# Kernel tuning notes

Measured on AMD Instinct MI355X. Metric: run time of the kernel, lower is better.

## Reference

```python
import jax, jax.numpy as jnp
import numpy as np

B, L, DIM = 16, 1024, 768
HEADS, DIM_HEAD = 12, 64
INNER = HEADS * DIM_HEAD  # 768


def _make_perm(key, l, dim):
    # first `dim` entries identity, rest a random permutation of [dim, l*dim)
    tail = dim + jax.random.permutation(key, (l - 1) * dim)
    return jnp.concatenate([jnp.arange(dim), tail]).astype(jnp.int32)


def setup_inputs() -> dict:
    key = jax.random.key(0)
    kx, kq, kk, kv, ko, kp1, kp2 = jax.random.split(key, 7)
    s = DIM ** -0.5
    return {
        "x": jax.random.normal(kx, (B, L, DIM), dtype=jnp.float32),
        "Wq": jax.random.normal(kq, (DIM, INNER), dtype=jnp.float32) * s,
        "Wk": jax.random.normal(kk, (DIM, INNER), dtype=jnp.float32) * s,
        "Wv": jax.random.normal(kv, (DIM, INNER), dtype=jnp.float32) * s,
        "Wo": jax.random.normal(ko, (INNER, DIM), dtype=jnp.float32) * (INNER ** -0.5),
        "bo": jnp.zeros((DIM,), dtype=jnp.float32),
        "permq": _make_perm(kp1, L, DIM),
        "permk": _make_perm(kp2, L, DIM),
    }


def reference(x, Wq, Wk, Wv, Wo, bo, permq, permk):
    b, l, d = x.shape
    scale = DIM_HEAD ** -0.5
    flat = x.reshape(b, l * d)
    xq = flat[:, permq].reshape(b, l, d)  # irregular gather across (seq*dim)
    xk = flat[:, permk].reshape(b, l, d)
    # projections + head split: b n (h d) -> b h n d
    q = (xq @ Wq).reshape(b, l, HEADS, DIM_HEAD).transpose(0, 2, 1, 3)
    k = (xk @ Wk).reshape(b, l, HEADS, DIM_HEAD).transpose(0, 2, 1, 3)
    v = (x @ Wv).reshape(b, l, HEADS, DIM_HEAD).transpose(0, 2, 1, 3)
    dots = jnp.einsum('bhnd,bhmd->bhnm', q, k) * scale
    attn = jax.nn.softmax(dots, axis=-1)
    out = jnp.einsum('bhnm,bhmd->bhnd', attn, v)
    out = out.transpose(0, 2, 1, 3).reshape(b, l, INNER)
    return out @ Wo + bo
```

## Files before the change

kernel.cpp:

```cpp
#include <hip/hip_runtime.h>

typedef unsigned short u16;
typedef __attribute__((ext_vector_type(8))) short bf16x8;
typedef __attribute__((ext_vector_type(4))) float f32x4;
typedef __attribute__((ext_vector_type(16))) float f32x16;

#define MFMA16(a, b, c) __builtin_amdgcn_mfma_f32_16x16x32_bf16(a, b, c, 0, 0, 0)
#define MFMA32(a, b, c) __builtin_amdgcn_mfma_f32_32x32x16_bf16(a, b, c, 0, 0, 0)

#if defined(__has_builtin)
# if __has_builtin(__builtin_amdgcn_cvt_pk_bf16_f32)
#  define HAS_CVT_PK 1
# else
#  define HAS_CVT_PK 0
# endif
#else
# define HAS_CVT_PK 0
#endif

__device__ __forceinline__ u16 f2b(float f) {
    union { float f; unsigned int u; } v;
    v.f = f;
    unsigned int u = v.u;
    return (u16)((u + 0x7fffu + ((u >> 16) & 1u)) >> 16);
}

__device__ __forceinline__ unsigned int f2b_pk(float a, float b) {
#if HAS_CVT_PK
    auto r = __builtin_amdgcn_cvt_pk_bf16_f32(a, b);
    unsigned int u;
    __builtin_memcpy(&u, &r, 4);
    return u;
#else
    return (unsigned int)f2b(a) | ((unsigned int)f2b(b) << 16);
#endif
}

__device__ __forceinline__ unsigned int cvtpk_asm(float a, float b) {
    unsigned int r;
    asm("v_cvt_pk_bf16_f32 %0, %1, %2" : "=v"(r) : "v"(a), "v"(b));
    return r;
}

__device__ __forceinline__ void g2l16(const u16* gsrc, u16* ldst) {
    __builtin_amdgcn_global_load_lds(
        (const __attribute__((address_space(1))) void*)gsrc,
        (__attribute__((address_space(3))) void*)ldst,
        16, 0, 0);
}

__global__ __launch_bounds__(256) void prep_weights(
    const float* __restrict__ Wq, const float* __restrict__ Wk,
    const float* __restrict__ Wv, const float* __restrict__ Wo,
    u16* __restrict__ wqt, u16* __restrict__ wkt,
    u16* __restrict__ wvt, u16* __restrict__ wot) {
    int id = blockIdx.x * 256 + threadIdx.x;
    int k = id / 768, n = id % 768;
    int t = n * 768 + k;
    wqt[t] = f2b(Wq[id] * (0.125f * 1.44269504088896340736f));
    wkt[t] = f2b(Wk[id]);
    wvt[t] = f2b(Wv[id]);
    wot[t] = f2b(Wo[id]);
}

__global__ __launch_bounds__(256) void cast_transpose(
    const float* __restrict__ x, u16* __restrict__ xb, u16* __restrict__ xT) {
    __shared__ __attribute__((aligned(16))) u16 T[16 * 1032];
    int t = threadIdx.x;
    int j0 = blockIdx.x * 1024;
#pragma unroll
    for (int b = 0; b < 16; ++b) {
        float4 v = *(const float4*)&x[(size_t)b * 786432 + j0 + 4 * t];
        uint2 o = make_uint2(f2b_pk(v.x, v.y), f2b_pk(v.z, v.w));
        *(uint2*)&T[b * 1032 + 4 * t] = o;
        *(uint2*)&xb[(size_t)b * 786432 + j0 + 4 * t] = o;
    }
    __syncthreads();
#pragma unroll
    for (int p = 0; p < 4; ++p) {
        int jl = t + 256 * p;
        union { u16 u[16]; int4 v[2]; } r;
#pragma unroll
        for (int b = 0; b < 16; ++b) r.u[b] = T[b * 1032 + jl];
        size_t base = (size_t)(j0 + jl) * 16;
        *(int4*)&xT[base] = r.v[0];
        *(int4*)&xT[base + 8] = r.v[1];
    }
}

__global__ __launch_bounds__(256) void gather_untranspose(
    const u16* __restrict__ xT, const int* __restrict__ permq,
    const int* __restrict__ permk, u16* __restrict__ dstQ,
    u16* __restrict__ dstK) {
    __shared__ u16 T[16 * 1034];
    const int* perm = blockIdx.y ? permk : permq;
    u16* dst = blockIdx.y ? dstK : dstQ;
    int t = threadIdx.x;
    int j0 = blockIdx.x * 1024;
#pragma unroll
    for (int p = 0; p < 4; ++p) {
        int jl = p * 256 + t;
        int pq = perm[j0 + jl];
        union { u16 u[16]; int4 v[2]; } r;
        const int4* s = (const int4*)&xT[(size_t)pq * 16];
        r.v[0] = s[0];
        r.v[1] = s[1];
#pragma unroll
        for (int b = 0; b < 16; ++b) T[b * 1034 + jl] = r.u[b];
    }
    __syncthreads();
#pragma unroll
    for (int b = 0; b < 16; ++b) {
        const unsigned int* s = (const unsigned int*)&T[b * 1034 + 4 * t];
        uint2 o = make_uint2(s[0], s[1]);
        *(uint2*)&dst[(size_t)b * 786432 + j0 + 4 * t] = o;
    }
}

__device__ __forceinline__ void gemm_core(
    const u16* __restrict__ A, const u16* __restrict__ Bt,
    u16* __restrict__ Cb, float* __restrict__ Cf,
    const float* __restrict__ bias, int m0, int n0, int K, int N, int mode) {
    __shared__ __attribute__((aligned(16))) u16 As[128 * 64];
    __shared__ __attribute__((aligned(16))) u16 Bs[128 * 64];
    int tid = threadIdx.x;
    int wave = tid >> 6, lane = tid & 63;
    int lo = lane & 15, quad = lane >> 4;
    int wm = (wave >> 1) * 64, wn = (wave & 1) * 64;
    f32x4 acc[4][4] = {};

    const u16* pA[4];
    const u16* pB[4];
    u16* lA[4];
    u16* lB[4];
#pragma unroll
    for (int p = 0; p < 4; ++p) {
        int c = p * 256 + wave * 64 + lane;
        int row = c >> 3;
        int scol = ((c & 7) ^ (row & 7)) * 8;
        pA[p] = A + (size_t)(m0 + row) * K + scol;
        pB[p] = Bt + (size_t)(n0 + row) * K + scol;
        lA[p] = &As[(p * 256 + wave * 64) * 8];
        lB[p] = &Bs[(p * 256 + wave * 64) * 8];
    }

    for (int k0 = 0; k0 < K; k0 += 64) {
        __syncthreads();
#pragma unroll
        for (int p = 0; p < 4; ++p) g2l16(pA[p], lA[p]);
#pragma unroll
        for (int p = 0; p < 4; ++p) g2l16(pB[p], lB[p]);
#pragma unroll
        for (int p = 0; p < 4; ++p) { pA[p] += 64; pB[p] += 64; }
        __syncthreads();
#pragma unroll
        for (int kk = 0; kk < 2; ++kk) {
            bf16x8 af[4], bf[4];
#pragma unroll
            for (int mi = 0; mi < 4; ++mi) {
                int row = wm + mi * 16 + lo;
                af[mi] = *(const bf16x8*)&As[row * 64 + (((kk << 2) | quad) ^ (lo & 7)) * 8];
            }
#pragma unroll
            for (int nj = 0; nj < 4; ++nj) {
                int row = wn + nj * 16 + lo;
                bf[nj] = *(const bf16x8*)&Bs[row * 64 + (((kk << 2) | quad) ^ (lo & 7)) * 8];
            }
#pragma unroll
            for (int mi = 0; mi < 4; ++mi)
#pragma unroll
                for (int nj = 0; nj < 4; ++nj)
                    acc[mi][nj] = MFMA16(af[mi], bf[nj], acc[mi][nj]);
        }
    }
#pragma unroll
    for (int mi = 0; mi < 4; ++mi)
#pragma unroll
        for (int nj = 0; nj < 4; ++nj) {
            int col = n0 + wn + nj * 16 + lo;
#pragma unroll
            for (int r = 0; r < 4; ++r) {
                int row = m0 + wm + mi * 16 + quad * 4 + r;
                float v = acc[mi][nj][r];
                if (mode) Cf[(size_t)row * N + col] = v + bias[col];
                else      Cb[(size_t)row * N + col] = f2b(v);
            }
        }
}

__global__ __launch_bounds__(256) void gemm_qkv(
    const u16* __restrict__ xqb, const u16* __restrict__ wqt, u16* __restrict__ Qb,
    const u16* __restrict__ xkb, const u16* __restrict__ wkt, u16* __restrict__ Kb,
    const u16* __restrict__ xb,  const u16* __restrict__ wvt, u16* __restrict__ Vb) {
    int id = blockIdx.x;
    int xcd = id & 7, slot = id >> 3;
    int gi = slot / 6, j = slot % 6;
    int group = xcd + 8 * gi;
    int my = group & 127, z = group >> 7;
    const u16* A = (z == 0) ? xqb : (z == 1) ? xkb : xb;
    const u16* W = (z == 0) ? wqt : (z == 1) ? wkt : wvt;
    u16* C = (z == 0) ? Qb : (z == 1) ? Kb : Vb;
    gemm_core(A, W, C, nullptr, nullptr, my * 128, j * 128, 768, 768, 0);
}

__global__ __launch_bounds__(256) void gemm_out(
    const u16* __restrict__ A, const u16* __restrict__ Bt,
    float* __restrict__ Cf, const float* __restrict__ bias) {
    int id = blockIdx.x;
    int xcd = id & 7, slot = id >> 3;
    int gi = slot / 6, j = slot % 6;
    int group = xcd + 8 * gi;
    gemm_core(A, Bt, nullptr, Cf, bias, group * 128, j * 128, 768, 768, 1);
}

#define LDA 72
__global__ __launch_bounds__(256) void transpose_v(
    const u16* __restrict__ Vb, u16* __restrict__ Vt) {
    __shared__ __attribute__((aligned(16))) u16 tile[64 * LDA];
    int lt = blockIdx.x;
    int bh = blockIdx.y;
    int b = bh / 12, h = bh % 12;
    int tid = threadIdx.x;
    int row = tid >> 3, co = (tid & 7) * 8;
#pragma unroll
    for (int p = 0; p < 2; ++p) {
        int r2 = row + p * 32;
        *(int4*)&tile[r2 * LDA + co] =
            *(const int4*)&Vb[(size_t)(b * 1024 + lt * 64 + r2) * 768 + h * 64 + co];
    }
    __syncthreads();
    int d = tid >> 2, nc = (tid & 3) * 16;
    union { u16 u[16]; int4 v[2]; } tt;
#pragma unroll
    for (int j = 0; j < 16; ++j)
        tt.u[j] = tile[(nc + j) * LDA + d];
    size_t base = ((size_t)bh * 64 + d) * 1024 + lt * 64 + nc;
    *(int4*)&Vt[base] = tt.v[0];
    *(int4*)&Vt[base + 8] = tt.v[1];
}

#define LDK 72
__global__ __launch_bounds__(256) void flash_attn(
    const u16* __restrict__ Qb, const u16* __restrict__ Kb,
    const u16* __restrict__ Vt, u16* __restrict__ AO) {
    __shared__ __attribute__((aligned(16))) u16 Ks[64 * LDK];
    __shared__ __attribute__((aligned(16))) u16 Vs[64 * LDK];
    int id = blockIdx.x;
    int bh = (id & 7) + ((id >> 6) << 3);
    int qt = (id >> 3) & 7;
    int b = bh / 12, h = bh % 12;
    int tid = threadIdx.x, wave = tid >> 6, lane = tid & 63;
    int ln = lane & 31, hi = lane >> 5;
    int q0 = qt * 128;

    bf16x8 qa[4];
    {
        const u16* qrow = &Qb[(size_t)(b * 1024 + q0 + wave * 32 + ln) * 768 + h * 64 + hi * 8];
#pragma unroll
        for (int kk = 0; kk < 4; ++kk)
            qa[kk] = *(const bf16x8*)&qrow[kk * 16];
    }

    const float M2 = 24.0f;
    float l_own = 0.0f;
    f32x16 acc_o[2] = {};
    const size_t kbase = (size_t)b * 1024 * 768 + h * 64;
    const size_t vbase = (size_t)bh * 64 * 1024;
    int srow = tid >> 3, sco = (tid & 7) * 8;

    int4 kr0 = *(const int4*)&Kb[kbase + (size_t)srow * 768 + sco];
    int4 kr1 = *(const int4*)&Kb[kbase + (size_t)(srow + 32) * 768 + sco];
    int4 vr0 = *(const int4*)&Vt[vbase + (size_t)srow * 1024 + sco];
    int4 vr1 = *(const int4*)&Vt[vbase + (size_t)(srow + 32) * 1024 + sco];

    for (int t = 0; t < 16; ++t) {
        __syncthreads();
        *(int4*)&Ks[srow * LDK + sco] = kr0;
        *(int4*)&Ks[(srow + 32) * LDK + sco] = kr1;
        *(int4*)&Vs[srow * LDK + sco] = vr0;
        *(int4*)&Vs[(srow + 32) * LDK + sco] = vr1;
        __syncthreads();
        int tn = (t + 1) & 15;
        kr0 = *(const int4*)&Kb[kbase + (size_t)(tn * 64 + srow) * 768 + sco];
        kr1 = *(const int4*)&Kb[kbase + (size_t)(tn * 64 + srow + 32) * 768 + sco];
        vr0 = *(const int4*)&Vt[vbase + (size_t)srow * 1024 + tn * 64 + sco];
        vr1 = *(const int4*)&Vt[vbase + (size_t)(srow + 32) * 1024 + tn * 64 + sco];
        f32x16 sacc[2] = {};
#pragma unroll
        for (int nj = 0; nj < 2; ++nj)
#pragma unroll
            for (int kk = 0; kk < 4; ++kk) {
                bf16x8 kb = *(const bf16x8*)&Ks[(ln + 32 * nj) * LDK + kk * 16 + hi * 8];
                sacc[nj] = MFMA32(kb, qa[kk], sacc[nj]);
            }
#pragma unroll
        for (int nj = 0; nj < 2; ++nj) {
            float p[16];
#pragma unroll
            for (int r = 0; r < 16; ++r)
                p[r] = __builtin_amdgcn_exp2f(sacc[nj][r] - M2);
            l_own += (((p[0] + p[1]) + (p[2] + p[3])) + ((p[4] + p[5]) + (p[6] + p[7])))
                   + (((p[8] + p[9]) + (p[10] + p[11])) + ((p[12] + p[13]) + (p[14] + p[15])));
            unsigned int c[8];
#pragma unroll
            for (int m = 0; m < 8; ++m)
                c[m] = cvtpk_asm(p[2 * m], p[2 * m + 1]);
            asm("v_permlane32_swap_b32 %0, %1" : "+v"(c[0]), "+v"(c[2]));
            asm("v_permlane32_swap_b32 %0, %1" : "+v"(c[1]), "+v"(c[3]));
            asm("v_permlane32_swap_b32 %0, %1" : "+v"(c[4]), "+v"(c[6]));
            asm("v_permlane32_swap_b32 %0, %1" : "+v"(c[5]), "+v"(c[7]));
            union { unsigned int w[4]; bf16x8 v; } pa0, pa1;
            pa0.w[0] = c[0]; pa0.w[1] = c[1]; pa0.w[2] = c[2]; pa0.w[3] = c[3];
            pa1.w[0] = c[4]; pa1.w[1] = c[5]; pa1.w[2] = c[6]; pa1.w[3] = c[7];
#pragma unroll
            for (int njd = 0; njd < 2; ++njd) {
                bf16x8 vb0 = *(const bf16x8*)&Vs[(ln + 32 * njd) * LDK + (2 * nj) * 16 + hi * 8];
                acc_o[njd] = MFMA32(pa0.v, vb0, acc_o[njd]);
            }
#pragma unroll
            for (int njd = 0; njd < 2; ++njd) {
                bf16x8 vb1 = *(const bf16x8*)&Vs[(ln + 32 * njd) * LDK + (2 * nj + 1) * 16 + hi * 8];
                acc_o[njd] = MFMA32(pa1.v, vb1, acc_o[njd]);
            }
        }
    }
    float l = l_own + __shfl_xor(l_own, 32, 64);
    float inv = 1.0f / l;
#pragma unroll
    for (int r = 0; r < 16; ++r) {
        int qrow = (r & 3) + 8 * (r >> 2) + 4 * hi;
        float invq = __shfl(inv, qrow, 64);
        int row = b * 1024 + q0 + wave * 32 + qrow;
#pragma unroll
        for (int njd = 0; njd < 2; ++njd)
            AO[(size_t)row * 768 + h * 64 + ln + 32 * njd] = f2b(acc_o[njd][r] * invq);
    }
}

static const size_t SZ_W  = (size_t)768 * 768 * 2;
static const size_t SZ_X  = (size_t)16 * 1024 * 768 * 2;
static const size_t OFF_WQT = 0;
static const size_t OFF_WKT = SZ_W;
static const size_t OFF_WVT = 2 * SZ_W;
static const size_t OFF_WOT = 3 * SZ_W;
static const size_t OFF_XB  = 4 * SZ_W;
static const size_t OFF_XQB = OFF_XB  + SZ_X;
static const size_t OFF_XKB = OFF_XQB + SZ_X;
static const size_t OFF_QB  = OFF_XKB + SZ_X;
static const size_t OFF_KB  = OFF_QB  + SZ_X;
static const size_t OFF_VB  = OFF_KB  + SZ_X;
static const size_t OFF_XT  = OFF_QB;
static const size_t OFF_VT  = OFF_XQB;
static const size_t OFF_AO  = OFF_XKB;

extern "C" void kernel_launch(void* const* d_in, const int* in_sizes, int n_in,
                              void* d_out, int out_size, void* d_ws, size_t ws_size,
                              hipStream_t stream) {
    const float* x  = (const float*)d_in[0];
    const float* Wq = (const float*)d_in[1];
    const float* Wk = (const float*)d_in[2];
    const float* Wv = (const float*)d_in[3];
    const float* Wo = (const float*)d_in[4];
    const float* bo = (const float*)d_in[5];
    const int* permq = (const int*)d_in[6];
    const int* permk = (const int*)d_in[7];
    float* out = (float*)d_out;
    char* ws = (char*)d_ws;
    u16* wqt = (u16*)(ws + OFF_WQT);
    u16* wkt = (u16*)(ws + OFF_WKT);
    u16* wvt = (u16*)(ws + OFF_WVT);
    u16* wot = (u16*)(ws + OFF_WOT);
    u16* xb  = (u16*)(ws + OFF_XB);
    u16* xqb = (u16*)(ws + OFF_XQB);
    u16* xkb = (u16*)(ws + OFF_XKB);
    u16* Qb  = (u16*)(ws + OFF_QB);
    u16* Kb  = (u16*)(ws + OFF_KB);
    u16* Vb  = (u16*)(ws + OFF_VB);
    u16* xT  = (u16*)(ws + OFF_XT);
    u16* Vt  = (u16*)(ws + OFF_VT);
    u16* AO  = (u16*)(ws + OFF_AO);

    prep_weights<<<2304, 256, 0, stream>>>(Wq, Wk, Wv, Wo, wqt, wkt, wvt, wot);
    cast_transpose<<<768, 256, 0, stream>>>(x, xb, xT);
    gather_untranspose<<<dim3(768, 2), 256, 0, stream>>>(xT, permq, permk, xqb, xkb);
    gemm_qkv<<<2304, 256, 0, stream>>>(xqb, wqt, Qb, xkb, wkt, Kb, xb, wvt, Vb);
    transpose_v<<<dim3(16, 192), 256, 0, stream>>>(Vb, Vt);
    flash_attn<<<1536, 256, 0, stream>>>(Qb, Kb, Vt, AO);
    gemm_out<<<768, 256, 0, stream>>>(AO, wot, out, bo);
}
```

Before: 362.9 us.

## Fuse V transpose into QKV GEMM epilogue and double-buffer flash K/V tiles

The V projection GEMM now writes its output directly in the per-head transposed layout (b,h,d,l), which removes the separate transpose_v kernel and its extra read and write of V. The flash attention kernel double-buffers its K/V shared-memory tiles, so one __syncthreads per iteration is dropped. The cost is that the transposed epilogue writes 8-byte chunks strided across l, which may coalesce worse, and shared memory per block doubles.

After: 371.0 us. 1.02x slower.

```diff
diff --git a/kernel.cpp b/kernel.cpp
--- a/kernel.cpp
+++ b/kernel.cpp
@@ -173,6 +173,22 @@
                     acc[mi][nj] = MFMA16(af[mi], bf[nj], acc[mi][nj]);
         }
     }
+    if (mode == 2) {
+#pragma unroll
+        for (int mi = 0; mi < 4; ++mi)
+#pragma unroll
+            for (int nj = 0; nj < 4; ++nj) {
+                int col = n0 + wn + nj * 16 + lo;
+                int h = col >> 6, d = col & 63;
+                int row0 = m0 + wm + mi * 16 + quad * 4;
+                int bq = row0 >> 10, l = row0 & 1023;
+                union { u16 u[4]; uint2 v2; } o;
+#pragma unroll
+                for (int r = 0; r < 4; ++r) o.u[r] = f2b(acc[mi][nj][r]);
+                *(uint2*)&Cb[((size_t)((bq * 12 + h) * 64 + d)) * 1024 + l] = o.v2;
+            }
+        return;
+    }
 #pragma unroll
     for (int mi = 0; mi < 4; ++mi)
 #pragma unroll
@@ -191,7 +207,7 @@
 __global__ __launch_bounds__(256) void gemm_qkv(
     const u16* __restrict__ xqb, const u16* __restrict__ wqt, u16* __restrict__ Qb,
     const u16* __restrict__ xkb, const u16* __restrict__ wkt, u16* __restrict__ Kb,
-    const u16* __restrict__ xb,  const u16* __restrict__ wvt, u16* __restrict__ Vb) {
+    const u16* __restrict__ xb,  const u16* __restrict__ wvt, u16* __restrict__ Vt) {
     int id = blockIdx.x;
     int xcd = id & 7, slot = id >> 3;
     int gi = slot / 6, j = slot % 6;
@@ -199,8 +215,9 @@
     int my = group & 127, z = group >> 7;
     const u16* A = (z == 0) ? xqb : (z == 1) ? xkb : xb;
     const u16* W = (z == 0) ? wqt : (z == 1) ? wkt : wvt;
-    u16* C = (z == 0) ? Qb : (z == 1) ? Kb : Vb;
-    gemm_core(A, W, C, nullptr, nullptr, my * 128, j * 128, 768, 768, 0);
+    u16* C = (z == 0) ? Qb : (z == 1) ? Kb : Vt;
+    gemm_core(A, W, C, nullptr, nullptr, my * 128, j * 128, 768, 768,
+              (z == 2) ? 2 : 0);
 }
 
 __global__ __launch_bounds__(256) void gemm_out(
@@ -213,38 +230,12 @@
     gemm_core(A, Bt, nullptr, Cf, bias, group * 128, j * 128, 768, 768, 1);
 }
 
-#define LDA 72
-__global__ __launch_bounds__(256) void transpose_v(
-    const u16* __restrict__ Vb, u16* __restrict__ Vt) {
-    __shared__ __attribute__((aligned(16))) u16 tile[64 * LDA];
-    int lt = blockIdx.x;
-    int bh = blockIdx.y;
-    int b = bh / 12, h = bh % 12;
-    int tid = threadIdx.x;
-    int row = tid >> 3, co = (tid & 7) * 8;
-#pragma unroll
-    for (int p = 0; p < 2; ++p) {
-        int r2 = row + p * 32;
-        *(int4*)&tile[r2 * LDA + co] =
-            *(const int4*)&Vb[(size_t)(b * 1024 + lt * 64 + r2) * 768 + h * 64 + co];
-    }
-    __syncthreads();
-    int d = tid >> 2, nc = (tid & 3) * 16;
-    union { u16 u[16]; int4 v[2]; } tt;
-#pragma unroll
-    for (int j = 0; j < 16; ++j)
-        tt.u[j] = tile[(nc + j) * LDA + d];
-    size_t base = ((size_t)bh * 64 + d) * 1024 + lt * 64 + nc;
-    *(int4*)&Vt[base] = tt.v[0];
-    *(int4*)&Vt[base + 8] = tt.v[1];
-}
-
 #define LDK 72
 __global__ __launch_bounds__(256) void flash_attn(
     const u16* __restrict__ Qb, const u16* __restrict__ Kb,
     const u16* __restrict__ Vt, u16* __restrict__ AO) {
-    __shared__ __attribute__((aligned(16))) u16 Ks[64 * LDK];
-    __shared__ __attribute__((aligned(16))) u16 Vs[64 * LDK];
+    __shared__ __attribute__((aligned(16))) u16 Ks[2][64 * LDK];
+    __shared__ __attribute__((aligned(16))) u16 Vs[2][64 * LDK];
     int id = blockIdx.x;
     int bh = (id & 7) + ((id >> 6) << 3);
     int qt = (id >> 3) & 7;
@@ -274,11 +265,12 @@
     int4 vr1 = *(const int4*)&Vt[vbase + (size_t)(srow + 32) * 1024 + sco];
 
     for (int t = 0; t < 16; ++t) {
-        __syncthreads();
-        *(int4*)&Ks[srow * LDK + sco] = kr0;
-        *(int4*)&Ks[(srow + 32) * LDK + sco] = kr1;
-        *(int4*)&Vs[srow * LDK + sco] = vr0;
-        *(int4*)&Vs[(srow + 32) * LDK + sco] = vr1;
+        u16* ks = Ks[t & 1];
+        u16* vs = Vs[t & 1];
+        *(int4*)&ks[srow * LDK + sco] = kr0;
+        *(int4*)&ks[(srow + 32) * LDK + sco] = kr1;
+        *(int4*)&vs[srow * LDK + sco] = vr0;
+        *(int4*)&vs[(srow + 32) * LDK + sco] = vr1;
         __syncthreads();
         int tn = (t + 1) & 15;
         kr0 = *(const int4*)&Kb[kbase + (size_t)(tn * 64 + srow) * 768 + sco];
@@ -290,7 +282,7 @@
         for (int nj = 0; nj < 2; ++nj)
 #pragma unroll
             for (int kk = 0; kk < 4; ++kk) {
-                bf16x8 kb = *(const bf16x8*)&Ks[(ln + 32 * nj) * LDK + kk * 16 + hi * 8];
+                bf16x8 kb = *(const bf16x8*)&ks[(ln + 32 * nj) * LDK + kk * 16 + hi * 8];
                 sacc[nj] = MFMA32(kb, qa[kk], sacc[nj]);
             }
 #pragma unroll
@@ -314,12 +306,12 @@
             pa1.w[0] = c[4]; pa1.w[1] = c[5]; pa1.w[2] = c[6]; pa1.w[3] = c[7];
 #pragma unroll
             for (int njd = 0; njd < 2; ++njd) {
-                bf16x8 vb0 = *(const bf16x8*)&Vs[(ln + 32 * njd) * LDK + (2 * nj) * 16 + hi * 8];
+                bf16x8 vb0 = *(const bf16x8*)&vs[(ln + 32 * njd) * LDK + (2 * nj) * 16 + hi * 8];
                 acc_o[njd] = MFMA32(pa0.v, vb0, acc_o[njd]);
             }
 #pragma unroll
             for (int njd = 0; njd < 2; ++njd) {
-                bf16x8 vb1 = *(const bf16x8*)&Vs[(ln + 32 * njd) * LDK + (2 * nj + 1) * 16 + hi * 8];
+                bf16x8 vb1 = *(const bf16x8*)&vs[(ln + 32 * njd) * LDK + (2 * nj + 1) * 16 + hi * 8];
                 acc_o[njd] = MFMA32(pa1.v, vb1, acc_o[njd]);
             }
         }
@@ -348,9 +340,8 @@
 static const size_t OFF_XKB = OFF_XQB + SZ_X;
 static const size_t OFF_QB  = OFF_XKB + SZ_X;
 static const size_t OFF_KB  = OFF_QB  + SZ_X;
-static const size_t OFF_VB  = OFF_KB  + SZ_X;
+static const size_t OFF_VT  = OFF_KB  + SZ_X;
 static const size_t OFF_XT  = OFF_QB;
-static const size_t OFF_VT  = OFF_XQB;
 static const size_t OFF_AO  = OFF_XKB;
 
 extern "C" void kernel_launch(void* const* d_in, const int* in_sizes, int n_in,
@@ -375,16 +366,14 @@
     u16* xkb = (u16*)(ws + OFF_XKB);
     u16* Qb  = (u16*)(ws + OFF_QB);
     u16* Kb  = (u16*)(ws + OFF_KB);
-    u16* Vb  = (u16*)(ws + OFF_VB);
+    u16* Vt  = (u16*)(ws + OFF_VT);
     u16* xT  = (u16*)(ws + OFF_XT);
-    u16* Vt  = (u16*)(ws + OFF_VT);
     u16* AO  = (u16*)(ws + OFF_AO);
 
     prep_weights<<<2304, 256, 0, stream>>>(Wq, Wk, Wv, Wo, wqt, wkt, wvt, wot);
     cast_transpose<<<768, 256, 0, stream>>>(x, xb, xT);
     gather_untranspose<<<dim3(768, 2), 256, 0, stream>>>(xT, permq, permk, xqb, xkb);
-    gemm_qkv<<<2304, 256, 0, stream>>>(xqb, wqt, Qb, xkb, wkt, Kb, xb, wvt, Vb);
-    transpose_v<<<dim3(16, 192), 256, 0, stream>>>(Vb, Vt);
+    gemm_qkv<<<2304, 256, 0, stream>>>(xqb, wqt, Qb, xkb, wkt, Kb, xb, wvt, Vt);
     flash_attn<<<1536, 256, 0, stream>>>(Qb, Kb, Vt, AO);
     gemm_out<<<768, 256, 0, stream>>>(AO, wot, out, bo);
 }
```
